# Performance work log

Measured on AMD Instinct MI355X. Metric: run time of the kernel, lower is better.

Reference implementation:

```python
import jax, jax.numpy as jnp
import numpy as np

H = 16  # num_heads (inner_dim 1024 // default head_dim 64)
D = 64  # head_dim
EPS = 1e-5

def layernorm(x, w, b):
    mu = jnp.mean(x, axis=-1, keepdims=True)
    var = jnp.var(x, axis=-1, keepdims=True)
    return (x - mu) * jax.lax.rsqrt(var + EPS) * w + b

def attention(x, kv, wq, wk, wv, wo, bo):
    b, t, c = x.shape
    s = kv.shape[1]
    q = (x @ wq).reshape(b, t, H, D).transpose(0, 2, 1, 3)   # bhtd
    k = (kv @ wk).reshape(b, s, H, D).transpose(0, 2, 1, 3)  # bhsd
    v = (kv @ wv).reshape(b, s, H, D).transpose(0, 2, 1, 3)
    scores = jnp.einsum('bhqd,bhkd->bhqk', q, k) * (D ** -0.5)
    attn = jax.nn.softmax(scores, axis=-1)
    out = jnp.einsum('bhqk,bhkd->bhqd', attn, v)
    out = out.transpose(0, 2, 1, 3).reshape(b, t, c)
    return out @ wo + bo

def setup_inputs() -> dict:
    key = jax.random.key(0)
    ks = jax.random.split(key, 16)
    hs = 1024
    dff = 4 * hs  # 4096
    sc = lambda fan_in: 1.0 / np.sqrt(fan_in)
    inp = {
        'x': jax.random.normal(ks[0], (2, 2048, hs), jnp.float32),
        'encoder_hidden_states': jax.random.normal(ks[1], (2, 512, 64), jnp.float32),
        'ln1_w': jnp.ones((hs,), jnp.float32), 'ln1_b': jnp.zeros((hs,), jnp.float32),
        'a1_wq': jax.random.normal(ks[2], (hs, hs), jnp.float32) * sc(hs),
        'a1_wk': jax.random.normal(ks[3], (hs, hs), jnp.float32) * sc(hs),
        'a1_wv': jax.random.normal(ks[4], (hs, hs), jnp.float32) * sc(hs),
        'a1_wo': jax.random.normal(ks[5], (hs, hs), jnp.float32) * sc(hs),
        'a1_bo': jnp.zeros((hs,), jnp.float32),
        'ln2_w': jnp.ones((hs,), jnp.float32), 'ln2_b': jnp.zeros((hs,), jnp.float32),
        'a2_wq': jax.random.normal(ks[6], (hs, hs), jnp.float32) * sc(hs),
        'a2_wk': jax.random.normal(ks[7], (64, hs), jnp.float32) * sc(64),
        'a2_wv': jax.random.normal(ks[8], (64, hs), jnp.float32) * sc(64),
        'a2_wo': jax.random.normal(ks[9], (hs, hs), jnp.float32) * sc(hs),
        'a2_bo': jnp.zeros((hs,), jnp.float32),
        'ln3_w': jnp.ones((hs,), jnp.float32), 'ln3_b': jnp.zeros((hs,), jnp.float32),
        'ff_w1': jax.random.normal(ks[10], (hs, 2 * dff), jnp.float32) * sc(hs),
        'ff_b1': jnp.zeros((2 * dff,), jnp.float32),
        'ff_w2': jax.random.normal(ks[11], (dff, hs), jnp.float32) * sc(dff),
        'ff_b2': jnp.zeros((hs,), jnp.float32),
    }
    return inp

def reference(x, encoder_hidden_states, ln1_w, ln1_b, a1_wq, a1_wk, a1_wv, a1_wo, a1_bo,
              ln2_w, ln2_b, a2_wq, a2_wk, a2_wv, a2_wo, a2_bo,
              ln3_w, ln3_b, ff_w1, ff_b1, ff_w2, ff_b2):
    # self-attention sub-block
    h = layernorm(x, ln1_w, ln1_b)
    x = x + attention(h, h, a1_wq, a1_wk, a1_wv, a1_wo, a1_bo)
    # cross-attention sub-block (kv from encoder_hidden_states, dim 64)
    h = layernorm(x, ln2_w, ln2_b)
    x = x + attention(h, encoder_hidden_states, a2_wq, a2_wk, a2_wv, a2_wo, a2_bo)
    # GEGLU feed-forward sub-block
    h = layernorm(x, ln3_w, ln3_b)
    hp = h @ ff_w1 + ff_b1
    h1, h2 = jnp.split(hp, 2, axis=-1)
    h = (h1 * jax.nn.gelu(h2, approximate=False)) @ ff_w2 + ff_b2
    return x + h
```

## Files before the change

kernel.cpp:

```cpp
#include <hip/hip_runtime.h>
#include <hip/hip_bf16.h>
#include <stdint.h>

typedef unsigned short u16;
typedef __bf16 bf16x8 __attribute__((ext_vector_type(8)));
typedef float f32x4 __attribute__((ext_vector_type(4)));
typedef u16 u16x8 __attribute__((ext_vector_type(8)));
typedef u16 u16x4 __attribute__((ext_vector_type(4)));

__device__ __forceinline__ u16 f2bf(float f) {
  union { float f; uint32_t u; } v; v.f = f;
  uint32_t r = v.u + 0x7fffu + ((v.u >> 16) & 1u);
  return (u16)(r >> 16);
}
__device__ __forceinline__ float bf2f(u16 u) {
  union { uint32_t u; float f; } v; v.u = ((uint32_t)u) << 16;
  return v.f;
}
__device__ __forceinline__ uint32_t cvtpk(float a, float b) {
  uint32_t r;
  asm("v_cvt_pk_bf16_f32 %0, %1, %2" : "=v"(r) : "v"(a), "v"(b));
  return r;
}

__device__ __forceinline__ void gld16(const u16* g, u16* l) {
  __builtin_amdgcn_global_load_lds(
      (const __attribute__((address_space(1))) uint32_t*)g,
      (__attribute__((address_space(3))) uint32_t*)l, 16, 0, 0);
}

__device__ __forceinline__ void stage_half(const u16* __restrict__ gbase, int ldg,
                                           u16* lbase, int tid) {
#pragma unroll
  for (int j = 0; j < 2; ++j) {
    const int idx = j * 512 + tid;
    const int row = idx >> 3, c8 = idx & 7;
    gld16(gbase + (size_t)row * ldg + ((c8 ^ (row & 7)) << 3), lbase + idx * 8);
  }
}

__global__ void wconv_t(const float* __restrict__ W, u16* __restrict__ Wt, int K, int N,
                        float scale) {
  __shared__ float tile[32][33];
  const int n0 = blockIdx.x * 32, k0 = blockIdx.y * 32;
  const int tx = threadIdx.x, ty = threadIdx.y;
#pragma unroll
  for (int i = 0; i < 4; ++i)
    tile[ty + 8 * i][tx] = W[(size_t)(k0 + ty + 8 * i) * N + n0 + tx];
  __syncthreads();
#pragma unroll
  for (int i = 0; i < 4; ++i)
    Wt[(size_t)(n0 + ty + 8 * i) * K + k0 + tx] = f2bf(scale * tile[tx][ty + 8 * i]);
}

__global__ void cvt_bf(const float* __restrict__ in, u16* __restrict__ out, int n) {
  int i = blockIdx.x * 256 + threadIdx.x;
  if (i < n) out[i] = f2bf(in[i]);
}

__global__ __launch_bounds__(256)
void ln_fwd(const float* __restrict__ X, const float* __restrict__ wt,
            const float* __restrict__ bs, u16* __restrict__ Y) {
  const int row = blockIdx.x, t = threadIdx.x;
  const float4 v = *(const float4*)&X[(size_t)row * 1024 + t * 4];
  float s = v.x + v.y + v.z + v.w;
  float s2 = v.x * v.x + v.y * v.y + v.z * v.z + v.w * v.w;
#pragma unroll
  for (int off = 32; off > 0; off >>= 1) {
    s += __shfl_xor(s, off);
    s2 += __shfl_xor(s2, off);
  }
  __shared__ float rs[4], rs2[4];
  const int w = t >> 6;
  if ((t & 63) == 0) { rs[w] = s; rs2[w] = s2; }
  __syncthreads();
  s = rs[0] + rs[1] + rs[2] + rs[3];
  s2 = rs2[0] + rs2[1] + rs2[2] + rs2[3];
  const float mu = s * (1.0f / 1024.0f);
  const float var = s2 * (1.0f / 1024.0f) - mu * mu;
  const float rstd = rsqrtf(var + 1e-5f);
  const float4 wv = *(const float4*)&wt[t * 4];
  const float4 bv = *(const float4*)&bs[t * 4];
  u16x4 o;
  o[0] = f2bf((v.x - mu) * rstd * wv.x + bv.x);
  o[1] = f2bf((v.y - mu) * rstd * wv.y + bv.y);
  o[2] = f2bf((v.z - mu) * rstd * wv.z + bv.z);
  o[3] = f2bf((v.w - mu) * rstd * wv.w + bv.w);
  *(u16x4*)&Y[(size_t)row * 1024 + t * 4] = o;
}

template<int TN>
__global__ __launch_bounds__(256, 2)
void gemm_bf16(const u16* __restrict__ A, int lda, const u16* __restrict__ Bt,
               int M, int N, int K, const float* __restrict__ bias,
               const float* __restrict__ resid, float oscale,
               float* __restrict__ outF, u16* __restrict__ outB) {
  constexpr int WNV = (TN == 128) ? 2 : 1;
  constexpr int WMV = 4 / WNV;
  constexpr int WM = 128 / WMV;
  constexpr int WN = TN / WNV;
  constexpr int MI = WM / 16, NI = WN / 16;
  __shared__ __align__(16) u16 Al[128 * 64];
  __shared__ __align__(16) u16 Bl[TN * 64];
  const int tid = threadIdx.x;
  const int w = tid >> 6, l = tid & 63, lo = l & 15, g = l >> 4;
  const int bm = blockIdx.x * 128, bn = blockIdx.y * TN;
  const int wm = (w / WNV) * WM, wn = (w % WNV) * WN;
  f32x4 acc[MI][NI] = {};

  for (int k0 = 0; k0 < K; k0 += 64) {
#pragma unroll
    for (int p = 0; p < 4; ++p) {
      int idx = p * 256 + tid;
      int row = idx >> 3, c = idx & 7;
      gld16(A + (size_t)(bm + row) * lda + k0 + c * 8, &Al[idx * 8]);
    }
#pragma unroll
    for (int p = 0; p < TN / 32; ++p) {
      int idx = p * 256 + tid;
      int row = idx >> 3, c = idx & 7;
      gld16(Bt + (size_t)(bn + row) * K + k0 + c * 8, &Bl[idx * 8]);
    }
    asm volatile("s_waitcnt vmcnt(0)" ::: "memory");
    __syncthreads();
#pragma unroll
    for (int ks = 0; ks < 2; ++ks) {
      bf16x8 af[MI], bf[NI];
#pragma unroll
      for (int i = 0; i < MI; ++i)
        af[i] = *(const bf16x8*)&Al[(wm + i * 16 + lo) * 64 + ks * 32 + g * 8];
#pragma unroll
      for (int i = 0; i < NI; ++i)
        bf[i] = *(const bf16x8*)&Bl[(wn + i * 16 + lo) * 64 + ks * 32 + g * 8];
#pragma unroll
      for (int mi = 0; mi < MI; ++mi)
#pragma unroll
        for (int ni = 0; ni < NI; ++ni)
          acc[mi][ni] = __builtin_amdgcn_mfma_f32_16x16x32_bf16(af[mi], bf[ni], acc[mi][ni], 0, 0, 0);
    }
    __syncthreads();
  }

#pragma unroll
  for (int mi = 0; mi < MI; ++mi) {
#pragma unroll
    for (int ni = 0; ni < NI; ++ni) {
      const int col = bn + wn + ni * 16 + lo;
      const float bb = bias ? bias[col] : 0.0f;
      const int row0 = bm + wm + mi * 16 + g * 4;
#pragma unroll
      for (int r = 0; r < 4; ++r) {
        const size_t off = (size_t)(row0 + r) * N + col;
        float v = acc[mi][ni][r] * oscale + bb;
        if (resid) v += resid[off];
        if (outF) outF[off] = v;
        else outB[off] = f2bf(v);
      }
    }
  }
}

__global__ __launch_bounds__(512, 2)
void gemm256(const u16* __restrict__ A, int lda, const u16* __restrict__ Bt,
             int M, int N, int K, const float* __restrict__ bias,
             const float* __restrict__ resid, float oscale,
             float* __restrict__ outF, u16* __restrict__ outB) {
  __shared__ __align__(16) u16 sm[65536];
  const int tid = threadIdx.x;
  const int w = tid >> 6, l = tid & 63, lo = l & 15, g = l >> 4;
  const int wrow = w >> 2, wcol = w & 3;
  const int gx = gridDim.x;
  const int nwg = gx * gridDim.y;
  const int lin = blockIdx.y * gx + blockIdx.x;
  const int q = nwg >> 3, r = nwg & 7;
  const int xcd = lin & 7, pos = lin >> 3;
  const int sid = (xcd < r ? xcd * (q + 1) : r * (q + 1) + (xcd - r) * q) + pos;
  const int bm = (sid % gx) * 256, bn = (sid / gx) * 256;

  const int NT = K >> 6;
  const int swz = (lo & 7) << 3;
  f32x4 acc[8][4] = {};

  stage_half(Bt + (size_t)bn * K, K, sm + 16384, tid);
  stage_half(Bt + (size_t)(bn + 128) * K, K, sm + 16384 + 8192, tid);
  stage_half(A + (size_t)bm * lda, lda, sm, tid);
  stage_half(A + (size_t)(bm + 128) * lda, lda, sm + 8192, tid);
  if (NT > 1) {
    stage_half(Bt + (size_t)bn * K + 64, K, sm + 32768 + 16384, tid);
    stage_half(Bt + (size_t)(bn + 128) * K + 64, K, sm + 32768 + 16384 + 8192, tid);
    stage_half(A + (size_t)bm * lda + 64, lda, sm + 32768, tid);
  }
  asm volatile("s_waitcnt vmcnt(6)" ::: "memory");
  __builtin_amdgcn_s_barrier();

  for (int t = 0; t < NT; ++t) {
    u16* Ab_ = sm + (t & 1) * 32768;
    u16* Bb_ = Ab_ + 16384;
    bf16x8 a0[4][2], a1[4][2], bfr[4][2];
#pragma unroll
    for (int mf = 0; mf < 4; ++mf) {
      const int rowi = wrow * 128 + mf * 16 + lo;
#pragma unroll
      for (int kk = 0; kk < 2; ++kk)
        a0[mf][kk] = *(const bf16x8*)&Ab_[rowi * 64 + ((kk * 32 + g * 8) ^ swz)];
    }
#pragma unroll
    for (int nf = 0; nf < 4; ++nf) {
      const int rowi = wcol * 64 + nf * 16 + lo;
#pragma unroll
      for (int kk = 0; kk < 2; ++kk)
        bfr[nf][kk] = *(const bf16x8*)&Bb_[rowi * 64 + ((kk * 32 + g * 8) ^ swz)];
    }
    if (t + 1 < NT)
      stage_half(A + (size_t)(bm + 128) * lda + (t + 1) * 64, lda,
                 sm + ((t + 1) & 1) * 32768 + 8192, tid);
    __builtin_amdgcn_s_barrier();
    asm volatile("s_waitcnt lgkmcnt(0)" ::: "memory");
    __builtin_amdgcn_s_setprio(1);
#pragma unroll
    for (int mf = 0; mf < 4; ++mf)
#pragma unroll
      for (int nf = 0; nf < 2; ++nf)
#pragma unroll
        for (int kk = 0; kk < 2; ++kk)
          acc[mf][nf] = __builtin_amdgcn_mfma_f32_16x16x32_bf16(a0[mf][kk], bfr[nf][kk], acc[mf][nf], 0, 0, 0);
    __builtin_amdgcn_s_setprio(0);
    __builtin_amdgcn_s_barrier();
    if (t + 2 < NT)
      stage_half(Bt + (size_t)bn * K + (t + 2) * 64, K,
                 sm + (t & 1) * 32768 + 16384, tid);
    __builtin_amdgcn_s_barrier();
    __builtin_amdgcn_s_setprio(1);
#pragma unroll
    for (int mf = 0; mf < 4; ++mf)
#pragma unroll
      for (int nf = 2; nf < 4; ++nf)
#pragma unroll
        for (int kk = 0; kk < 2; ++kk)
          acc[mf][nf] = __builtin_amdgcn_mfma_f32_16x16x32_bf16(a0[mf][kk], bfr[nf][kk], acc[mf][nf], 0, 0, 0);
    __builtin_amdgcn_s_setprio(0);
    __builtin_amdgcn_s_barrier();
#pragma unroll
    for (int mf = 0; mf < 4; ++mf) {
      const int rowi = wrow * 128 + 64 + mf * 16 + lo;
#pragma unroll
      for (int kk = 0; kk < 2; ++kk)
        a1[mf][kk] = *(const bf16x8*)&Ab_[rowi * 64 + ((kk * 32 + g * 8) ^ swz)];
    }
    if (t + 2 < NT)
      stage_half(Bt + (size_t)(bn + 128) * K + (t + 2) * 64, K,
                 sm + (t & 1) * 32768 + 16384 + 8192, tid);
    __builtin_amdgcn_s_barrier();
    asm volatile("s_waitcnt lgkmcnt(0)" ::: "memory");
    __builtin_amdgcn_s_setprio(1);
#pragma unroll
    for (int mf = 0; mf < 4; ++mf)
#pragma unroll
      for (int nf = 0; nf < 2; ++nf)
#pragma unroll
        for (int kk = 0; kk < 2; ++kk)
          acc[4 + mf][nf] = __builtin_amdgcn_mfma_f32_16x16x32_bf16(a1[mf][kk], bfr[nf][kk], acc[4 + mf][nf], 0, 0, 0);
    __builtin_amdgcn_s_setprio(0);
    __builtin_amdgcn_s_barrier();
    if (t + 2 < NT)
      stage_half(A + (size_t)bm * lda + (t + 2) * 64, lda,
                 sm + (t & 1) * 32768, tid);
    __builtin_amdgcn_s_barrier();
    __builtin_amdgcn_s_setprio(1);
#pragma unroll
    for (int mf = 0; mf < 4; ++mf)
#pragma unroll
      for (int nf = 2; nf < 4; ++nf)
#pragma unroll
        for (int kk = 0; kk < 2; ++kk)
          acc[4 + mf][nf] = __builtin_amdgcn_mfma_f32_16x16x32_bf16(a1[mf][kk], bfr[nf][kk], acc[4 + mf][nf], 0, 0, 0);
    __builtin_amdgcn_s_setprio(0);
    asm volatile("s_waitcnt vmcnt(6)" ::: "memory");
    __builtin_amdgcn_s_barrier();
  }

#pragma unroll
  for (int mi = 0; mi < 8; ++mi) {
#pragma unroll
    for (int ni = 0; ni < 4; ++ni) {
      const int col = bn + wcol * 64 + ni * 16 + lo;
      const float bb = bias ? bias[col] : 0.0f;
      const int row0 = bm + wrow * 128 + mi * 16 + g * 4;
#pragma unroll
      for (int rr = 0; rr < 4; ++rr) {
        const size_t off = (size_t)(row0 + rr) * N + col;
        float v = acc[mi][ni][rr] * oscale + bb;
        if (resid) v += resid[off];
        if (outF) outF[off] = v;
        else outB[off] = f2bf(v);
      }
    }
  }
}

__global__ __launch_bounds__(256, 4)
void attn_fwd(const u16* __restrict__ Q, int ldq, const u16* __restrict__ K,
              const u16* __restrict__ V, int ldkv, u16* __restrict__ O,
              int T, int S) {
  __shared__ __align__(16) u16 Kl[64 * 64];
  __shared__ __align__(16) u16 Vt[64 * 64];
  const int tid = threadIdx.x, w = tid >> 6, l = tid & 63, lo = l & 15, g = l >> 4;
  const int nwg = gridDim.x * gridDim.y;
  const int n = blockIdx.y * gridDim.x + blockIdx.x;
  const int sid = (n & 7) * (nwg >> 3) + (n >> 3);
  const int qt = sid % gridDim.x, bh = sid / gridDim.x;
  const int b = bh >> 4, h = bh & 15, hc = h * 64;
  const int q0 = qt * 64 + w * 16;
  const size_t qrow = (size_t)b * T + q0;
  const size_t kvrow = (size_t)b * S;

  bf16x8 qf[2];
#pragma unroll
  for (int kk = 0; kk < 2; ++kk)
    qf[kk] = *(const bf16x8*)&Q[(qrow + lo) * ldq + hc + kk * 32 + g * 8];

  f32x4 oa[4] = {};
  float m = -1e30f, lsum = 0.0f;

  const int krow = tid >> 3;
  const int kcol = (((tid & 7) ^ (krow & 7)) << 3);
  const int vk = tid >> 2, vdq = (tid & 3) * 16;
  const int pos_k = ((vk >> 5) << 5) | (((vk >> 2) & 3) << 3) |
                    (((vk >> 4) & 1) << 2) | (vk & 3);

  const int ntile = S >> 6;
  for (int t0 = 0; t0 < ntile; ++t0) {
    __syncthreads();
#pragma unroll
    for (int c = 0; c < 2; ++c)
      gld16(K + (kvrow + t0 * 64 + c * 32 + krow) * ldkv + hc + kcol,
            &Kl[c * 2048 + tid * 8]);
    {
      const size_t vg = (kvrow + t0 * 64 + vk) * ldkv + hc + vdq;
      u16x8 v1 = *(const u16x8*)&V[vg];
      u16x8 v2 = *(const u16x8*)&V[vg + 8];
#pragma unroll
      for (int j = 0; j < 8; ++j) {
        const int d1 = vdq + j, d2 = vdq + 8 + j;
        Vt[d1 * 64 + (pos_k ^ ((d1 & 7) << 3))] = v1[j];
        Vt[d2 * 64 + (pos_k ^ ((d2 & 7) << 3))] = v2[j];
      }
    }
    asm volatile("s_waitcnt vmcnt(0)" ::: "memory");
    __syncthreads();

    f32x4 s[4] = {};
#pragma unroll
    for (int c = 0; c < 4; ++c)
#pragma unroll
      for (int kk = 0; kk < 2; ++kk) {
        bf16x8 kf = *(const bf16x8*)&Kl[(c * 16 + lo) * 64 +
                                        ((kk * 32 + g * 8) ^ ((lo & 7) << 3))];
        s[c] = __builtin_amdgcn_mfma_f32_16x16x32_bf16(kf, qf[kk], s[c], 0, 0, 0);
      }

    float mx = fmaxf(fmaxf(fmaxf(s[0][0], s[0][1]), fmaxf(s[0][2], s[0][3])),
                     fmaxf(fmaxf(s[1][0], s[1][1]), fmaxf(s[1][2], s[1][3])));
    mx = fmaxf(mx, fmaxf(fmaxf(fmaxf(s[2][0], s[2][1]), fmaxf(s[2][2], s[2][3])),
                         fmaxf(fmaxf(s[3][0], s[3][1]), fmaxf(s[3][2], s[3][3]))));
    mx = fmaxf(mx, __shfl_xor(mx, 16));
    mx = fmaxf(mx, __shfl_xor(mx, 32));
    const float mn = fmaxf(m, mx);
    const float al = exp2f(m - mn);
    m = mn;
    float psum = 0.0f;
#pragma unroll
    for (int c = 0; c < 4; ++c)
#pragma unroll
      for (int r = 0; r < 4; ++r) {
        s[c][r] = exp2f(s[c][r] - mn);
        psum += s[c][r];
      }
    psum += __shfl_xor(psum, 16);
    psum += __shfl_xor(psum, 32);
    lsum = lsum * al + psum;
    f32x4 arv;
#pragma unroll
    for (int r = 0; r < 4; ++r) arv[r] = __shfl(al, 20 * g + r);
#pragma unroll
    for (int dn = 0; dn < 4; ++dn) oa[dn] *= arv;

    union { uint32_t u[4]; bf16x8 v; } af[2];
#pragma unroll
    for (int ks = 0; ks < 2; ++ks) {
      af[ks].u[0] = cvtpk(s[2 * ks][0], s[2 * ks][1]);
      af[ks].u[1] = cvtpk(s[2 * ks][2], s[2 * ks][3]);
      af[ks].u[2] = cvtpk(s[2 * ks + 1][0], s[2 * ks + 1][1]);
      af[ks].u[3] = cvtpk(s[2 * ks + 1][2], s[2 * ks + 1][3]);
    }
#pragma unroll
    for (int dn = 0; dn < 4; ++dn)
#pragma unroll
      for (int ks = 0; ks < 2; ++ks) {
        bf16x8 vf = *(const bf16x8*)&Vt[(dn * 16 + lo) * 64 +
                                        ((ks * 32 + g * 8) ^ ((lo & 7) << 3))];
        oa[dn] = __builtin_amdgcn_mfma_f32_16x16x32_bf16(af[ks].v, vf, oa[dn], 0, 0, 0);
      }
  }

  const float il = 1.0f / lsum;
  float ir[4];
#pragma unroll
  for (int r = 0; r < 4; ++r) ir[r] = __shfl(il, 20 * g + r);
#pragma unroll
  for (int dn = 0; dn < 4; ++dn)
#pragma unroll
    for (int r = 0; r < 4; ++r)
      O[(qrow + g * 4 + r) * 1024 + hc + dn * 16 + lo] = f2bf(oa[dn][r] * ir[r]);
}

__global__ __launch_bounds__(256)
void geglu_k(u16* __restrict__ hp) {
  const size_t i = (size_t)blockIdx.x * 256 + threadIdx.x;
  const int row = (int)(i >> 9), c8 = (int)(i & 511);
  u16* p1 = hp + (size_t)row * 8192 + c8 * 8;
  const u16* p2 = p1 + 4096;
  u16x8 a = *(const u16x8*)p1;
  u16x8 bq = *(const u16x8*)p2;
  u16x8 o;
#pragma unroll
  for (int j = 0; j < 8; ++j) {
    float x1 = bf2f(a[j]), x2 = bf2f(bq[j]);
    float ge = 0.5f * x2 * (1.0f + erff(x2 * 0.70710678118f));
    o[j] = f2bf(x1 * ge);
  }
  *(u16x8*)p1 = o;
}

extern "C" void kernel_launch(void* const* d_in, const int* in_sizes, int n_in,
                              void* d_out, int out_size, void* d_ws, size_t ws_size,
                              hipStream_t stream) {
  const float* x      = (const float*)d_in[0];
  const float* enc    = (const float*)d_in[1];
  const float* ln1_w  = (const float*)d_in[2];
  const float* ln1_b  = (const float*)d_in[3];
  const float* a1_wq  = (const float*)d_in[4];
  const float* a1_wk  = (const float*)d_in[5];
  const float* a1_wv  = (const float*)d_in[6];
  const float* a1_wo  = (const float*)d_in[7];
  const float* a1_bo  = (const float*)d_in[8];
  const float* ln2_w  = (const float*)d_in[9];
  const float* ln2_b  = (const float*)d_in[10];
  const float* a2_wq  = (const float*)d_in[11];
  const float* a2_wk  = (const float*)d_in[12];
  const float* a2_wv  = (const float*)d_in[13];
  const float* a2_wo  = (const float*)d_in[14];
  const float* a2_bo  = (const float*)d_in[15];
  const float* ln3_w  = (const float*)d_in[16];
  const float* ln3_b  = (const float*)d_in[17];
  const float* ff_w1  = (const float*)d_in[18];
  const float* ff_b1  = (const float*)d_in[19];
  const float* ff_w2  = (const float*)d_in[20];
  const float* ff_b2  = (const float*)d_in[21];

  char* ws = (char*)d_ws;
  const size_t MB = 1u << 20;
  u16* wqkv1t = (u16*)(ws + 0 * MB);
  u16* wo1t   = (u16*)(ws + 6 * MB);
  u16* wq2t   = (u16*)(ws + 8 * MB);
  u16* wo2t   = (u16*)(ws + 10 * MB);
  u16* wk2t   = (u16*)(ws + 12 * MB);
  u16* wv2t   = (u16*)(ws + 12 * MB + 256 * 1024);
  u16* encb   = (u16*)(ws + 12 * MB + 512 * 1024);
  u16* w1t    = (u16*)(ws + 13 * MB);
  u16* w2t    = (u16*)(ws + 29 * MB);
  float* x2   = (float*)(ws + 37 * MB);
  u16* hbuf   = (u16*)(ws + 53 * MB);
  u16* qkv    = (u16*)(ws + 61 * MB);
  u16* Qb     = (u16*)(ws + 61 * MB);
  u16* Kb     = (u16*)(ws + 69 * MB);
  u16* Vb     = (u16*)(ws + 77 * MB);
  u16* Ab     = (u16*)(ws + 85 * MB);
  float* x1   = (float*)(ws + 93 * MB);
  u16* hp     = (u16*)(ws + 61 * MB);

  const float SCL = 0.125f * 1.44269504f;
  const dim3 tb(32, 8);
  wconv_t<<<dim3(32, 32), tb, 0, stream>>>(a1_wq, wqkv1t, 1024, 1024, SCL);
  wconv_t<<<dim3(32, 32), tb, 0, stream>>>(a1_wk, wqkv1t + 1024 * 1024, 1024, 1024, 1.0f);
  wconv_t<<<dim3(32, 32), tb, 0, stream>>>(a1_wv, wqkv1t + 2048 * 1024, 1024, 1024, 1.0f);
  wconv_t<<<dim3(32, 32), tb, 0, stream>>>(a1_wo, wo1t, 1024, 1024, 1.0f);
  wconv_t<<<dim3(32, 32), tb, 0, stream>>>(a2_wq, wq2t, 1024, 1024, SCL);
  wconv_t<<<dim3(32, 2),  tb, 0, stream>>>(a2_wk, wk2t, 64, 1024, 1.0f);
  wconv_t<<<dim3(32, 2),  tb, 0, stream>>>(a2_wv, wv2t, 64, 1024, 1.0f);
  wconv_t<<<dim3(32, 32), tb, 0, stream>>>(a2_wo, wo2t, 1024, 1024, 1.0f);
  wconv_t<<<dim3(256, 32), tb, 0, stream>>>(ff_w1, w1t, 1024, 8192, 1.0f);
  wconv_t<<<dim3(32, 128), tb, 0, stream>>>(ff_w2, w2t, 4096, 1024, 1.0f);
  cvt_bf<<<256, 256, 0, stream>>>(enc, encb, 2 * 512 * 64);

  ln_fwd<<<4096, 256, 0, stream>>>(x, ln1_w, ln1_b, hbuf);
  gemm256<<<dim3(16, 12), 512, 0, stream>>>(hbuf, 1024, wqkv1t, 4096, 3072, 1024, nullptr, nullptr, 1.0f, nullptr, qkv);
  attn_fwd<<<dim3(32, 32), 256, 0, stream>>>(qkv, 3072, qkv + 1024, qkv + 2048, 3072, Ab, 2048, 2048);
  gemm_bf16<64><<<dim3(32, 16), 256, 0, stream>>>(Ab, 1024, wo1t, 4096, 1024, 1024, a1_bo, x, 1.0f, x1, nullptr);

  ln_fwd<<<4096, 256, 0, stream>>>(x1, ln2_w, ln2_b, hbuf);
  gemm_bf16<64><<<dim3(32, 16), 256, 0, stream>>>(hbuf, 1024, wq2t, 4096, 1024, 1024, nullptr, nullptr, 1.0f, nullptr, Qb);
  gemm_bf16<64><<<dim3(8, 16), 256, 0, stream>>>(encb, 64, wk2t, 1024, 1024, 64, nullptr, nullptr, 1.0f, nullptr, Kb);
  gemm_bf16<64><<<dim3(8, 16), 256, 0, stream>>>(encb, 64, wv2t, 1024, 1024, 64, nullptr, nullptr, 1.0f, nullptr, Vb);
  attn_fwd<<<dim3(32, 32), 256, 0, stream>>>(Qb, 1024, Kb, Vb, 1024, Ab, 2048, 512);
  gemm_bf16<64><<<dim3(32, 16), 256, 0, stream>>>(Ab, 1024, wo2t, 4096, 1024, 1024, a2_bo, x1, 1.0f, x2, nullptr);

  ln_fwd<<<4096, 256, 0, stream>>>(x2, ln3_w, ln3_b, hbuf);
  gemm256<<<dim3(16, 32), 512, 0, stream>>>(hbuf, 1024, w1t, 4096, 8192, 1024, ff_b1, nullptr, 1.0f, nullptr, hp);
  geglu_k<<<8192, 256, 0, stream>>>(hp);
  gemm_bf16<64><<<dim3(32, 16), 256, 0, stream>>>(hp, 8192, w2t, 4096, 1024, 4096, ff_b2, x2, 1.0f, (float*)d_out, nullptr);
}
```

Measured before the change: 470.7 us.

## Pre-transpose V and double-buffer K/V tiles in attention with async loads

Adds a separate vtrans kernel that writes V in a per-head transposed, pre-permuted layout, so attention can fetch both K and V tiles with direct global-to-LDS loads instead of transposing V in registers on every tile. The attention loop now double-buffers the K and V tiles, prefetching the next tile while the current one is computed, in place of a synchronous load-then-compute loop. It also adds an XCD-aware block remap to gemm_bf16 and fixes the final-iteration vmcnt wait in gemm256. The cost is an extra kernel launch and an extra pass over V through global memory.

```diff
diff --git a/kernel.cpp b/kernel.cpp
--- a/kernel.cpp
+++ b/kernel.cpp
@@ -56,6 +56,31 @@
 __global__ void cvt_bf(const float* __restrict__ in, u16* __restrict__ out, int n) {
   int i = blockIdx.x * 256 + threadIdx.x;
   if (i < n) out[i] = f2bf(in[i]);
+}
+
+__global__ __launch_bounds__(256)
+void vtrans(const u16* __restrict__ V, int ldv, int hoff, u16* __restrict__ Vt, int S) {
+  __shared__ u16 tile[64][72];
+  const int t0 = blockIdx.x, bh = blockIdx.y;
+  const int b = bh >> 4, hc = (bh & 15) * 64 + hoff;
+  const int tid = threadIdx.x;
+  const int r = tid >> 2, dq = (tid & 3) * 16;
+  const int pos = ((r >> 5) << 5) | (((r >> 2) & 3) << 3) | (((r >> 4) & 1) << 2) | (r & 3);
+  const size_t grow = ((size_t)b * S + t0 * 64 + r) * ldv + hc + dq;
+  u16x8 v1 = *(const u16x8*)&V[grow];
+  u16x8 v2 = *(const u16x8*)&V[grow + 8];
+#pragma unroll
+  for (int j = 0; j < 8; ++j) {
+    tile[dq + j][pos] = v1[j];
+    tile[dq + 8 + j][pos] = v2[j];
+  }
+  __syncthreads();
+  const int d = tid >> 2, c = (tid & 3) * 16;
+  u16x8 o1, o2;
+#pragma unroll
+  for (int j = 0; j < 8; ++j) { o1[j] = tile[d][c + j]; o2[j] = tile[d][c + 8 + j]; }
+  *(u16x8*)&Vt[((size_t)bh * 64 + d) * S + t0 * 64 + c] = o1;
+  *(u16x8*)&Vt[((size_t)bh * 64 + d) * S + t0 * 64 + c + 8] = o2;
 }
 
 __global__ __launch_bounds__(256)
@@ -104,7 +129,12 @@
   __shared__ __align__(16) u16 Bl[TN * 64];
   const int tid = threadIdx.x;
   const int w = tid >> 6, l = tid & 63, lo = l & 15, g = l >> 4;
-  const int bm = blockIdx.x * 128, bn = blockIdx.y * TN;
+  const int gx = gridDim.x, nwg = gx * gridDim.y;
+  const int lin = blockIdx.y * gx + blockIdx.x;
+  const int q = nwg >> 3, r = nwg & 7;
+  const int xcd = lin & 7, pos = lin >> 3;
+  const int sid = (xcd < r ? xcd * (q + 1) : r * (q + 1) + (xcd - r) * q) + pos;
+  const int bm = (sid % gx) * 128, bn = (sid / gx) * TN;
   const int wm = (w / WNV) * WM, wn = (w % WNV) * WN;
   f32x4 acc[MI][NI] = {};
 
@@ -149,9 +179,9 @@
       const float bb = bias ? bias[col] : 0.0f;
       const int row0 = bm + wm + mi * 16 + g * 4;
 #pragma unroll
-      for (int r = 0; r < 4; ++r) {
-        const size_t off = (size_t)(row0 + r) * N + col;
-        float v = acc[mi][ni][r] * oscale + bb;
+      for (int rr = 0; rr < 4; ++rr) {
+        const size_t off = (size_t)(row0 + rr) * N + col;
+        float v = acc[mi][ni][rr] * oscale + bb;
         if (resid) v += resid[off];
         if (outF) outF[off] = v;
         else outB[off] = f2bf(v);
@@ -275,7 +305,8 @@
         for (int kk = 0; kk < 2; ++kk)
           acc[4 + mf][nf] = __builtin_amdgcn_mfma_f32_16x16x32_bf16(a1[mf][kk], bfr[nf][kk], acc[4 + mf][nf], 0, 0, 0);
     __builtin_amdgcn_s_setprio(0);
-    asm volatile("s_waitcnt vmcnt(6)" ::: "memory");
+    if (t + 2 < NT) asm volatile("s_waitcnt vmcnt(6)" ::: "memory");
+    else            asm volatile("s_waitcnt vmcnt(0)" ::: "memory");
     __builtin_amdgcn_s_barrier();
   }
 
@@ -299,11 +330,10 @@
 }
 
 __global__ __launch_bounds__(256, 4)
-void attn_fwd(const u16* __restrict__ Q, int ldq, const u16* __restrict__ K,
-              const u16* __restrict__ V, int ldkv, u16* __restrict__ O,
-              int T, int S) {
-  __shared__ __align__(16) u16 Kl[64 * 64];
-  __shared__ __align__(16) u16 Vt[64 * 64];
+void attn_fwd(const u16* __restrict__ Q, int ldq, const u16* __restrict__ K, int ldk,
+              const u16* __restrict__ Vt, u16* __restrict__ O, int T, int S) {
+  __shared__ __align__(16) u16 Kl[2][4096];
+  __shared__ __align__(16) u16 Vl[2][4096];
   const int tid = threadIdx.x, w = tid >> 6, l = tid & 63, lo = l & 15, g = l >> 4;
   const int nwg = gridDim.x * gridDim.y;
   const int n = blockIdx.y * gridDim.x + blockIdx.x;
@@ -312,7 +342,8 @@
   const int b = bh >> 4, h = bh & 15, hc = h * 64;
   const int q0 = qt * 64 + w * 16;
   const size_t qrow = (size_t)b * T + q0;
-  const size_t kvrow = (size_t)b * S;
+  const size_t krow0 = (size_t)b * S;
+  const size_t vrow0 = (size_t)bh * 64;
 
   bf16x8 qf[2];
 #pragma unroll
@@ -322,40 +353,42 @@
   f32x4 oa[4] = {};
   float m = -1e30f, lsum = 0.0f;
 
-  const int krow = tid >> 3;
-  const int kcol = (((tid & 7) ^ (krow & 7)) << 3);
-  const int vk = tid >> 2, vdq = (tid & 3) * 16;
-  const int pos_k = ((vk >> 5) << 5) | (((vk >> 2) & 3) << 3) |
-                    (((vk >> 4) & 1) << 2) | (vk & 3);
+  const int srow = tid >> 3;
+  const int scol = (((tid & 7) ^ (srow & 7)) << 3);
 
   const int ntile = S >> 6;
+#pragma unroll
+  for (int c = 0; c < 2; ++c)
+    gld16(K + (krow0 + c * 32 + srow) * ldk + hc + scol, &Kl[0][c * 2048 + tid * 8]);
+#pragma unroll
+  for (int c = 0; c < 2; ++c)
+    gld16(Vt + (vrow0 + c * 32 + srow) * S + scol, &Vl[0][c * 2048 + tid * 8]);
+
   for (int t0 = 0; t0 < ntile; ++t0) {
-    __syncthreads();
-#pragma unroll
-    for (int c = 0; c < 2; ++c)
-      gld16(K + (kvrow + t0 * 64 + c * 32 + krow) * ldkv + hc + kcol,
-            &Kl[c * 2048 + tid * 8]);
-    {
-      const size_t vg = (kvrow + t0 * 64 + vk) * ldkv + hc + vdq;
-      u16x8 v1 = *(const u16x8*)&V[vg];
-      u16x8 v2 = *(const u16x8*)&V[vg + 8];
-#pragma unroll
-      for (int j = 0; j < 8; ++j) {
-        const int d1 = vdq + j, d2 = vdq + 8 + j;
-        Vt[d1 * 64 + (pos_k ^ ((d1 & 7) << 3))] = v1[j];
-        Vt[d2 * 64 + (pos_k ^ ((d2 & 7) << 3))] = v2[j];
-      }
-    }
-    asm volatile("s_waitcnt vmcnt(0)" ::: "memory");
-    __syncthreads();
+    const int cur = t0 & 1;
+    if (t0 + 1 < ntile) {
+      const int nxt = cur ^ 1;
+#pragma unroll
+      for (int c = 0; c < 2; ++c)
+        gld16(K + (krow0 + (t0 + 1) * 64 + c * 32 + srow) * ldk + hc + scol,
+              &Kl[nxt][c * 2048 + tid * 8]);
+#pragma unroll
+      for (int c = 0; c < 2; ++c)
+        gld16(Vt + (vrow0 + c * 32 + srow) * S + (t0 + 1) * 64 + scol,
+              &Vl[nxt][c * 2048 + tid * 8]);
+      asm volatile("s_waitcnt vmcnt(4)" ::: "memory");
+    } else {
+      asm volatile("s_waitcnt vmcnt(0)" ::: "memory");
+    }
+    __builtin_amdgcn_s_barrier();
 
     f32x4 s[4] = {};
 #pragma unroll
     for (int c = 0; c < 4; ++c)
 #pragma unroll
       for (int kk = 0; kk < 2; ++kk) {
-        bf16x8 kf = *(const bf16x8*)&Kl[(c * 16 + lo) * 64 +
-                                        ((kk * 32 + g * 8) ^ ((lo & 7) << 3))];
+        bf16x8 kf = *(const bf16x8*)&Kl[cur][(c * 16 + lo) * 64 +
+                                            ((kk * 32 + g * 8) ^ ((lo & 7) << 3))];
         s[c] = __builtin_amdgcn_mfma_f32_16x16x32_bf16(kf, qf[kk], s[c], 0, 0, 0);
       }
 
@@ -372,16 +405,16 @@
 #pragma unroll
     for (int c = 0; c < 4; ++c)
 #pragma unroll
-      for (int r = 0; r < 4; ++r) {
-        s[c][r] = exp2f(s[c][r] - mn);
-        psum += s[c][r];
+      for (int rr = 0; rr < 4; ++rr) {
+        s[c][rr] = exp2f(s[c][rr] - mn);
+        psum += s[c][rr];
       }
     psum += __shfl_xor(psum, 16);
     psum += __shfl_xor(psum, 32);
     lsum = lsum * al + psum;
     f32x4 arv;
 #pragma unroll
-    for (int r = 0; r < 4; ++r) arv[r] = __shfl(al, 20 * g + r);
+    for (int rr = 0; rr < 4; ++rr) arv[rr] = __shfl(al, 20 * g + rr);
 #pragma unroll
     for (int dn = 0; dn < 4; ++dn) oa[dn] *= arv;
 
@@ -397,21 +430,23 @@
     for (int dn = 0; dn < 4; ++dn)
 #pragma unroll
       for (int ks = 0; ks < 2; ++ks) {
-        bf16x8 vf = *(const bf16x8*)&Vt[(dn * 16 + lo) * 64 +
-                                        ((ks * 32 + g * 8) ^ ((lo & 7) << 3))];
+        bf16x8 vf = *(const bf16x8*)&Vl[cur][(dn * 16 + lo) * 64 +
+                                            ((ks * 32 + g * 8) ^ ((lo & 7) << 3))];
         oa[dn] = __builtin_amdgcn_mfma_f32_16x16x32_bf16(af[ks].v, vf, oa[dn], 0, 0, 0);
       }
+    asm volatile("s_waitcnt lgkmcnt(0)" ::: "memory");
+    __builtin_amdgcn_s_barrier();
   }
 
   const float il = 1.0f / lsum;
   float ir[4];
 #pragma unroll
-  for (int r = 0; r < 4; ++r) ir[r] = __shfl(il, 20 * g + r);
+  for (int rr = 0; rr < 4; ++rr) ir[rr] = __shfl(il, 20 * g + rr);
 #pragma unroll
   for (int dn = 0; dn < 4; ++dn)
 #pragma unroll
-    for (int r = 0; r < 4; ++r)
-      O[(qrow + g * 4 + r) * 1024 + hc + dn * 16 + lo] = f2bf(oa[dn][r] * ir[r]);
+    for (int rr = 0; rr < 4; ++rr)
+      O[(qrow + g * 4 + rr) * 1024 + hc + dn * 16 + lo] = f2bf(oa[dn][rr] * ir[rr]);
 }
 
 __global__ __launch_bounds__(256)
@@ -470,6 +505,8 @@
   u16* w1t    = (u16*)(ws + 13 * MB);
   u16* w2t    = (u16*)(ws + 29 * MB);
   float* x2   = (float*)(ws + 37 * MB);
+  u16* Vt1    = (u16*)(ws + 37 * MB);
+  u16* Vt2    = (u16*)(ws + 45 * MB);
   u16* hbuf   = (u16*)(ws + 53 * MB);
   u16* qkv    = (u16*)(ws + 61 * MB);
   u16* Qb     = (u16*)(ws + 61 * MB);
@@ -495,14 +532,16 @@
 
   ln_fwd<<<4096, 256, 0, stream>>>(x, ln1_w, ln1_b, hbuf);
   gemm256<<<dim3(16, 12), 512, 0, stream>>>(hbuf, 1024, wqkv1t, 4096, 3072, 1024, nullptr, nullptr, 1.0f, nullptr, qkv);
-  attn_fwd<<<dim3(32, 32), 256, 0, stream>>>(qkv, 3072, qkv + 1024, qkv + 2048, 3072, Ab, 2048, 2048);
+  vtrans<<<dim3(32, 32), 256, 0, stream>>>(qkv, 3072, 2048, Vt1, 2048);
+  attn_fwd<<<dim3(32, 32), 256, 0, stream>>>(qkv, 3072, qkv + 1024, 3072, Vt1, Ab, 2048, 2048);
   gemm_bf16<64><<<dim3(32, 16), 256, 0, stream>>>(Ab, 1024, wo1t, 4096, 1024, 1024, a1_bo, x, 1.0f, x1, nullptr);
 
   ln_fwd<<<4096, 256, 0, stream>>>(x1, ln2_w, ln2_b, hbuf);
   gemm_bf16<64><<<dim3(32, 16), 256, 0, stream>>>(hbuf, 1024, wq2t, 4096, 1024, 1024, nullptr, nullptr, 1.0f, nullptr, Qb);
   gemm_bf16<64><<<dim3(8, 16), 256, 0, stream>>>(encb, 64, wk2t, 1024, 1024, 64, nullptr, nullptr, 1.0f, nullptr, Kb);
   gemm_bf16<64><<<dim3(8, 16), 256, 0, stream>>>(encb, 64, wv2t, 1024, 1024, 64, nullptr, nullptr, 1.0f, nullptr, Vb);
-  attn_fwd<<<dim3(32, 32), 256, 0, stream>>>(Qb, 1024, Kb, Vb, 1024, Ab, 2048, 512);
+  vtrans<<<dim3(8, 32), 256, 0, stream>>>(Vb, 1024, 0, Vt2, 512);
+  attn_fwd<<<dim3(32, 32), 256, 0, stream>>>(Qb, 1024, Kb, 1024, Vt2, Ab, 2048, 512);
   gemm_bf16<64><<<dim3(32, 16), 256, 0, stream>>>(Ab, 1024, wo2t, 4096, 1024, 1024, a2_bo, x1, 1.0f, x2, nullptr);
 
   ln_fwd<<<4096, 256, 0, stream>>>(x2, ln3_w, ln3_b, hbuf);
```

Result: no change. 479.3 us (+1.8%).
